# Optimization experiments

Hardware: AMD Instinct MI355X
Metric: run time of the kernel (lower is better)

The kernel has to match this reference:

```python
import jax, jax.numpy as jnp
import numpy as np

D_IN = 1024
D_OUT = 1024
NUM_HEADS = 16
HEAD_DIM = D_OUT // NUM_HEADS


def setup_inputs() -> dict:
    key = jax.random.key(0)
    ks = jax.random.split(key, 6)
    s = 0.02
    return {
        "x": jax.random.normal(ks[0], (4, 2048, D_IN), dtype=jnp.float32),
        "W_q": jax.random.normal(ks[1], (D_IN, D_OUT), dtype=jnp.float32) * s,
        "W_k": jax.random.normal(ks[2], (D_IN, D_OUT), dtype=jnp.float32) * s,
        "W_v": jax.random.normal(ks[3], (D_IN, D_OUT), dtype=jnp.float32) * s,
        "W_o": jax.random.normal(ks[4], (D_OUT, D_OUT), dtype=jnp.float32) * s,
        "b_o": jax.random.normal(ks[5], (D_OUT,), dtype=jnp.float32) * s,
    }


def reference(x, W_q, W_k, W_v, W_o, b_o):
    b, n, _ = x.shape
    # project and split heads: [b, h, n, d]
    q = (x @ W_q).reshape(b, n, NUM_HEADS, HEAD_DIM).transpose(0, 2, 1, 3)
    k = (x @ W_k).reshape(b, n, NUM_HEADS, HEAD_DIM).transpose(0, 2, 1, 3)
    v = (x @ W_v).reshape(b, n, NUM_HEADS, HEAD_DIM).transpose(0, 2, 1, 3)
    scores = jnp.einsum("bhqd,bhkd->bhqk", q, k)
    causal = jnp.tril(jnp.ones((n, n), dtype=bool))  # True = keep
    scores = jnp.where(causal, scores, -jnp.inf)
    attn = jax.nn.softmax(scores / np.sqrt(HEAD_DIM).astype(np.float32), axis=-1)
    ctx = jnp.einsum("bhqk,bhkd->bhqd", attn, v)
    ctx = ctx.transpose(0, 2, 1, 3).reshape(b, n, D_OUT)
    return ctx @ W_o + b_o
```

## Files before the change

kernel.cpp:

```cpp
#include <hip/hip_runtime.h>
#include <hip/hip_bf16.h>

#define NHEADS 16
#define HDIM 64
#define SEQ 2048
#define BATCH 4
#define DMODEL 1024
#define MTOT (BATCH * SEQ)

typedef short v8s __attribute__((ext_vector_type(8)));
typedef short v4s __attribute__((ext_vector_type(4)));
typedef float v4f __attribute__((ext_vector_type(4)));
typedef float v16f __attribute__((ext_vector_type(16)));
typedef unsigned int v4u __attribute__((ext_vector_type(4)));
typedef unsigned short u16;
typedef unsigned int u32;

__device__ __forceinline__ u16 f2bf(float f) {
    union { float f; unsigned u; } v; v.f = f;
    unsigned r = v.u + 0x7FFFu + ((v.u >> 16) & 1u);
    return (u16)(r >> 16);
}

__device__ __forceinline__ void g2l16(const u16* g, short* l) {
    __builtin_amdgcn_global_load_lds(
        (const __attribute__((address_space(1))) u32*)g,
        (__attribute__((address_space(3))) u32*)l, 16, 0, 0);
}

__device__ __forceinline__ unsigned pk_bf16(float a, float b) {
    unsigned r;
    asm("v_cvt_pk_bf16_f32 %0, %1, %2" : "=v"(r) : "v"(a), "v"(b));
    return r;
}
__device__ __forceinline__ void pl32swap(unsigned& x, unsigned& y) {
    asm("v_permlane32_swap_b32 %0, %1" : "+v"(x), "+v"(y));
}
__device__ __forceinline__ v8s build_pa(float a0, float a1, float a2, float a3,
                                        float b0, float b1, float b2, float b3) {
    unsigned X  = pk_bf16(a0, a1);
    unsigned X2 = pk_bf16(a2, a3);
    unsigned Y  = pk_bf16(b0, b1);
    unsigned Y2 = pk_bf16(b2, b3);
    pl32swap(X, Y);
    pl32swap(X2, Y2);
    v4u w; w[0] = X; w[1] = X2; w[2] = Y; w[3] = Y2;
    return __builtin_bit_cast(v8s, w);
}

__device__ __forceinline__ void transpose_body(
    const float* __restrict__ src, u16* __restrict__ dst, int k0, int n0)
{
    __shared__ __align__(8) short Ts[64 * 68];
    const int t = threadIdx.x;
    const int n4 = (t & 15) * 4, kl = t >> 4;
#pragma unroll
    for (int it = 0; it < 4; ++it) {
        int k = kl + 16 * it;
        v4f v = *(const v4f*)&src[(size_t)(k0 + k) * DMODEL + n0 + n4];
        v4s p;
#pragma unroll
        for (int e = 0; e < 4; ++e) p[e] = (short)f2bf(v[e]);
        *(v4s*)&Ts[k * 68 + n4] = p;
    }
    __syncthreads();
    const int nl = t >> 4, k4 = (t & 15) * 4;
#pragma unroll
    for (int it = 0; it < 4; ++it) {
        int n = nl + 16 * it;
        v4s o;
#pragma unroll
        for (int e = 0; e < 4; ++e) o[e] = Ts[(k4 + e) * 68 + n];
        *(v4s*)&dst[(size_t)(n0 + n) * DMODEL + k0 + k4] = o;
    }
}

__global__ __launch_bounds__(256)
void transpose_w(const float* __restrict__ src, u16* __restrict__ dst)
{
    transpose_body(src, dst, blockIdx.x * 64, blockIdx.y * 64);
}

__global__ __launch_bounds__(256)
void prep(const float* __restrict__ x, u16* __restrict__ xb,
          const float* __restrict__ s0, const float* __restrict__ s1,
          const float* __restrict__ s2, const float* __restrict__ s3,
          u16* __restrict__ wdst)
{
    const int blk = blockIdx.x;
    if (blk < 1024) {
        const int z = blk >> 8;
        const int rem = blk & 255;
        const float* src = (z == 0) ? s0 : (z == 1) ? s1 : (z == 2) ? s2 : s3;
        transpose_body(src, wdst + (size_t)z * DMODEL * DMODEL,
                       (rem & 15) * 64, (rem >> 4) * 64);
    } else {
        size_t i = ((size_t)(blk - 1024) * 256 + threadIdx.x) * 8;
        v4f a = *(const v4f*)&x[i];
        v4f b = *(const v4f*)&x[i + 4];
        v8s p;
#pragma unroll
        for (int e = 0; e < 4; ++e) p[e] = (short)f2bf(a[e]);
#pragma unroll
        for (int e = 0; e < 4; ++e) p[4 + e] = (short)f2bf(b[e]);
        *(v8s*)&xb[i] = p;
    }
}

#define QSCALE (0.125f * 1.44269504088896f)

#define QKV_ABUF (256 * 64)
#define QKV_BBUF (128 * 64)

__device__ __forceinline__ void qkv_stage3(
    const u16* __restrict__ xb, const u16* __restrict__ W,
    int m0, int t, int s, int part, short* As3, short* Bs3)
{
    const int srr = t >> 3;
    const int scol = ((t & 7) ^ (srr & 7)) * 8;
    short* A = As3 + (s % 3) * QKV_ABUF;
    short* B = Bs3 + (s % 3) * QKV_BBUF;
    const int k0 = s * 64;
    if (part == 0) {
        g2l16(&xb[(size_t)(m0 + srr) * DMODEL + k0 + scol], &A[t * 8]);
        g2l16(&xb[(size_t)(m0 + 64 + srr) * DMODEL + k0 + scol],
              &A[4096 + t * 8]);
        g2l16(&W[(size_t)srr * DMODEL + k0 + scol], &B[t * 8]);
    } else {
        g2l16(&xb[(size_t)(m0 + 128 + srr) * DMODEL + k0 + scol],
              &A[8192 + t * 8]);
        g2l16(&xb[(size_t)(m0 + 192 + srr) * DMODEL + k0 + scol],
              &A[12288 + t * 8]);
        g2l16(&W[(size_t)(64 + srr) * DMODEL + k0 + scol], &B[4096 + t * 8]);
    }
}

template <bool SW>
__device__ __forceinline__ void qkv_loop32(
    const u16* __restrict__ xb, const u16* __restrict__ W,
    int m0, int t, short* As3, short* Bs3, v16f (&acc)[2][2])
{
    const int lane = t & 63;
    const int l31 = lane & 31;
    const int hi = lane >> 5;
    const int wave = t >> 6;
    const int wm = (wave >> 1) * 64;
    const int wn = (wave & 1) * 64;
    const int x7 = l31 & 7;

    qkv_stage3(xb, W, m0, t, 0, 0, As3, Bs3);
    qkv_stage3(xb, W, m0, t, 0, 1, As3, Bs3);
    qkv_stage3(xb, W, m0, t, 1, 0, As3, Bs3);
    qkv_stage3(xb, W, m0, t, 1, 1, As3, Bs3);
    asm volatile("s_waitcnt vmcnt(6)" ::: "memory");
    __builtin_amdgcn_sched_barrier(0);
    __builtin_amdgcn_s_barrier();
    __builtin_amdgcn_sched_barrier(0);

#pragma unroll 1
    for (int tt = 0; tt < 16; ++tt) {
        const short* A = As3 + (tt % 3) * QKV_ABUF;
        const short* B = Bs3 + (tt % 3) * QKV_BBUF;
        v8s af[2][2], bf[2][2];

#pragma unroll
        for (int i = 0; i < 2; ++i)
#pragma unroll
            for (int ks = 0; ks < 2; ++ks) {
                af[i][ks] = *(const v8s*)&A[(wm + i * 32 + l31) * 64 +
                                            (((ks * 2 + hi) ^ x7) << 3)];
                bf[i][ks] = *(const v8s*)&B[(wn + i * 32 + l31) * 64 +
                                            (((ks * 2 + hi) ^ x7) << 3)];
            }
        if (tt + 2 < 16) qkv_stage3(xb, W, m0, t, tt + 2, 0, As3, Bs3);
        __builtin_amdgcn_s_barrier();
        asm volatile("s_waitcnt lgkmcnt(0)" ::: "memory");
        __builtin_amdgcn_sched_barrier(0);
        __builtin_amdgcn_s_setprio(1);
#pragma unroll
        for (int i = 0; i < 2; ++i)
#pragma unroll
            for (int j = 0; j < 2; ++j)
#pragma unroll
                for (int ks = 0; ks < 2; ++ks) {
                    if (SW)
                        acc[i][j] = __builtin_amdgcn_mfma_f32_32x32x16_bf16(
                            bf[j][ks], af[i][ks], acc[i][j], 0, 0, 0);
                    else
                        acc[i][j] = __builtin_amdgcn_mfma_f32_32x32x16_bf16(
                            af[i][ks], bf[j][ks], acc[i][j], 0, 0, 0);
                }
        __builtin_amdgcn_s_setprio(0);
        __builtin_amdgcn_s_barrier();

#pragma unroll
        for (int i = 0; i < 2; ++i)
#pragma unroll
            for (int ks = 0; ks < 2; ++ks) {
                af[i][ks] = *(const v8s*)&A[(wm + i * 32 + l31) * 64 +
                                            ((((ks + 2) * 2 + hi) ^ x7) << 3)];
                bf[i][ks] = *(const v8s*)&B[(wn + i * 32 + l31) * 64 +
                                            ((((ks + 2) * 2 + hi) ^ x7) << 3)];
            }
        if (tt + 2 < 16) qkv_stage3(xb, W, m0, t, tt + 2, 1, As3, Bs3);
        __builtin_amdgcn_s_barrier();
        asm volatile("s_waitcnt lgkmcnt(0)" ::: "memory");
        __builtin_amdgcn_sched_barrier(0);
        __builtin_amdgcn_s_setprio(1);
#pragma unroll
        for (int i = 0; i < 2; ++i)
#pragma unroll
            for (int j = 0; j < 2; ++j)
#pragma unroll
                for (int ks = 0; ks < 2; ++ks) {
                    if (SW)
                        acc[i][j] = __builtin_amdgcn_mfma_f32_32x32x16_bf16(
                            bf[j][ks], af[i][ks], acc[i][j], 0, 0, 0);
                    else
                        acc[i][j] = __builtin_amdgcn_mfma_f32_32x32x16_bf16(
                            af[i][ks], bf[j][ks], acc[i][j], 0, 0, 0);
                }
        __builtin_amdgcn_s_setprio(0);
        if (tt < 14)       asm volatile("s_waitcnt vmcnt(6)" ::: "memory");
        else if (tt == 14) asm volatile("s_waitcnt vmcnt(0)" ::: "memory");
        __builtin_amdgcn_sched_barrier(0);
        __builtin_amdgcn_s_barrier();
        __builtin_amdgcn_sched_barrier(0);
    }
}

__global__ __launch_bounds__(512, 1)
void qkv_fast(const u16* __restrict__ xb, const u16* __restrict__ Wt,
              u16* __restrict__ Qb, u16* __restrict__ Kb, u16* __restrict__ Vt)
{
    __shared__ __align__(16) short As3[3 * QKV_ABUF];
    __shared__ __align__(16) short Bs3[3 * QKV_BBUF];

    const int bx = blockIdx.x;
    const int which = bx >> 3;
    const int n0 = (bx & 7) * 128;
    const int m0 = blockIdx.y * 256;
    const u16* W = Wt + (size_t)which * DMODEL * DMODEL + (size_t)n0 * DMODEL;

    const int t = threadIdx.x;
    const int lane = t & 63;
    const int l31 = lane & 31;
    const int hi = lane >> 5;
    const int wave = t >> 6;
    const int wm = (wave >> 1) * 64;
    const int wn = (wave & 1) * 64;

    v16f acc[2][2];
#pragma unroll
    for (int i = 0; i < 2; ++i)
#pragma unroll
        for (int j = 0; j < 2; ++j)
#pragma unroll
            for (int r = 0; r < 16; ++r) acc[i][j][r] = 0.f;

    if (which == 2) {
        qkv_loop32<true>(xb, W, m0, t, As3, Bs3, acc);
#pragma unroll
        for (int i = 0; i < 2; ++i) {
            int m = m0 + wm + i * 32 + l31;
            int b = m >> 11, n = m & (SEQ - 1);
#pragma unroll
            for (int j = 0; j < 2; ++j)
#pragma unroll
                for (int r = 0; r < 16; ++r) {
                    int ncol = n0 + wn + j * 32 + (r & 3) + 8 * (r >> 2)
                               + 4 * hi;
                    int h = ncol >> 6, d = ncol & 63;
                    Vt[((size_t)(b * NHEADS + h) * HDIM + d) * SEQ + n] =
                        f2bf(acc[i][j][r]);
                }
        }
    } else {
        qkv_loop32<false>(xb, W, m0, t, As3, Bs3, acc);
        u16* Ob = which ? Kb : Qb;
        const float scale = which ? 1.0f : QSCALE;
#pragma unroll
        for (int j = 0; j < 2; ++j) {
            int col = n0 + wn + j * 32 + l31;
            int h = col >> 6, d = col & 63;
#pragma unroll
            for (int i = 0; i < 2; ++i)
#pragma unroll
                for (int r = 0; r < 16; ++r) {
                    int m = m0 + wm + i * 32 + (r & 3) + 8 * (r >> 2) + 4 * hi;
                    int b = m >> 11, n = m & (SEQ - 1);
                    Ob[((size_t)(b * NHEADS + h) * SEQ + n) * HDIM + d] =
                        f2bf(acc[i][j][r] * scale);
                }
        }
    }
}

__device__ __forceinline__ void qkv_epilogue(
    v4f (&acc)[4][4], int which, int n0, int m0, int wn, int wm,
    int l15, int quad, u16* Qb, u16* Kb, u16* Vt)
{
    if (which == 2) {
#pragma unroll
        for (int i = 0; i < 4; ++i)
#pragma unroll
            for (int j = 0; j < 4; ++j) {
                int col = n0 + wn + j * 16 + l15;
                int h = col >> 6, d = col & 63;
                int m = m0 + wm + i * 16 + quad * 4;
                int b = m >> 11, n = m & (SEQ - 1);
                v4s pv;
#pragma unroll
                for (int r = 0; r < 4; ++r) pv[r] = (short)f2bf(acc[i][j][r]);
                *(v4s*)&Vt[((size_t)(b * NHEADS + h) * HDIM + d) * SEQ + n] = pv;
            }
    } else {
        u16* Ob = (which == 0) ? Qb : Kb;
        const float scale = (which == 0) ? QSCALE : 1.0f;
#pragma unroll
        for (int i = 0; i < 4; ++i)
#pragma unroll
            for (int j = 0; j < 4; ++j) {
                int col = n0 + wn + j * 16 + l15;
                int h = col >> 6, d = col & 63;
#pragma unroll
                for (int r = 0; r < 4; ++r) {
                    int m = m0 + wm + i * 16 + quad * 4 + r;
                    int b = m >> 11, n = m & (SEQ - 1);
                    Ob[((size_t)(b * NHEADS + h) * SEQ + n) * HDIM + d] =
                        f2bf(acc[i][j][r] * scale);
                }
            }
    }
}

__global__ __launch_bounds__(256, 2)
void qkv_slow(const float* __restrict__ x, const u16* __restrict__ Wt,
              u16* __restrict__ Qb, u16* __restrict__ Kb, u16* __restrict__ Vt)
{
    __shared__ __align__(16) short As[128 * 32];
    __shared__ __align__(16) short Bs[128 * 32];

    const int which = blockIdx.z;
    const u16* W = Wt + (size_t)which * DMODEL * DMODEL;

    const int n0 = blockIdx.x * 128;
    const int m0 = blockIdx.y * 128;
    const int t = threadIdx.x;
    const int lane = t & 63;
    const int l15 = lane & 15;
    const int quad = lane >> 4;
    const int wave = t >> 6;
    const int wm = (wave >> 1) * 64;
    const int wn = (wave & 1) * 64;
    const int srow = t >> 2;
    const int sc8 = (t & 3) * 8;

    v4f acc[4][4];
#pragma unroll
    for (int i = 0; i < 4; ++i)
#pragma unroll
        for (int j = 0; j < 4; ++j) acc[i][j] = {0.f, 0.f, 0.f, 0.f};

    for (int k0 = 0; k0 < DMODEL; k0 += 32) {
        __syncthreads();
        g2l16(&W[(size_t)(n0 + srow) * DMODEL + k0 + sc8], &Bs[srow * 32 + sc8]);
        g2l16(&W[(size_t)(n0 + 64 + srow) * DMODEL + k0 + sc8],
              &Bs[(64 + srow) * 32 + sc8]);
#pragma unroll
        for (int it = 0; it < 2; ++it) {
            int row = srow + 64 * it;
            const float* xp = &x[(size_t)(m0 + row) * DMODEL + k0 + sc8];
            v4f x0 = *(const v4f*)xp;
            v4f x1 = *(const v4f*)(xp + 4);
            v8s av;
#pragma unroll
            for (int e = 0; e < 4; ++e) av[e] = (short)f2bf(x0[e]);
#pragma unroll
            for (int e = 0; e < 4; ++e) av[4 + e] = (short)f2bf(x1[e]);
            *(v8s*)&As[row * 32 + sc8] = av;
        }
        __syncthreads();

        v8s af[4], bf[4];
#pragma unroll
        for (int i = 0; i < 4; ++i)
            af[i] = *(const v8s*)&As[(wm + i * 16 + l15) * 32 + quad * 8];
#pragma unroll
        for (int j = 0; j < 4; ++j)
            bf[j] = *(const v8s*)&Bs[(wn + j * 16 + l15) * 32 + quad * 8];
#pragma unroll
        for (int i = 0; i < 4; ++i)
#pragma unroll
            for (int j = 0; j < 4; ++j)
                acc[i][j] = __builtin_amdgcn_mfma_f32_16x16x32_bf16(
                    af[i], bf[j], acc[i][j], 0, 0, 0);
    }
    qkv_epilogue(acc, which, n0, m0, wn, wm, l15, quad, Qb, Kb, Vt);
}

#define VXOR(d) ((((d) & 7) << 1) | (((d) >> 3) & 1))

__global__ __launch_bounds__(256, 2)
void attn(const u16* __restrict__ Qb, const u16* __restrict__ Kb,
          const u16* __restrict__ Vt, u16* __restrict__ Cx)
{
    __shared__ __align__(16) short Ks[2][128 * 64];
    __shared__ __align__(16) short Vs[2][64 * 128];

    const int ell = blockIdx.x;
    const int xcd = ell & 7;
    const int rest = ell >> 3;
    const int p = rest & 7;
    const int bh = ((rest >> 3) << 3) | xcd;

    const int t = threadIdx.x;
    const int lane = t & 63;
    const int l31 = lane & 31;
    const int hi = lane >> 5;
    const int wave = t >> 6;
    const int koff = hi * 8;

    const u16* Qh = Qb + (size_t)bh * SEQ * HDIM;
    const u16* Kh = Kb + (size_t)bh * SEQ * HDIM;
    const u16* Vh = Vt + (size_t)bh * HDIM * SEQ;

    const int krow = t >> 3;
    const int kslot = t & 7;
    const int vrow = t >> 4;
    const int vslot = t & 15;
    const int b = bh >> 4, h = bh & 15;

#pragma unroll 1
    for (int phase = 0; phase < 2; ++phase) {
        const int qt = phase ? p : (15 - p);
        const int q0w = qt * 128 + wave * 32;

        v8s qf[4];
#pragma unroll
        for (int dc = 0; dc < 4; ++dc)
            qf[dc] = *(const v8s*)
                &Qh[(size_t)(q0w + l31) * HDIM + dc * 16 + koff];

        v16f o0, o1;
#pragma unroll
        for (int r = 0; r < 16; ++r) { o0[r] = 0.f; o1[r] = 0.f; }
        float ls = 0.f;

        v8s pk[4], pv[4];
#pragma unroll
        for (int it = 0; it < 4; ++it)
            pk[it] = *(const v8s*)
                &Kh[(size_t)(it * 32 + krow) * HDIM + kslot * 8];
#pragma unroll
        for (int it = 0; it < 4; ++it)
            pv[it] = *(const v8s*)
                &Vh[(size_t)(it * 16 + vrow) * SEQ + vslot * 8];
#pragma unroll
        for (int it = 0; it < 4; ++it) {
            int row = it * 32 + krow;
            *(v8s*)&Ks[0][row * 64 + ((kslot ^ (row & 7)) << 3)] = pk[it];
        }
#pragma unroll
        for (int it = 0; it < 4; ++it) {
            int d = it * 16 + vrow;
            *(v8s*)&Vs[0][d * 128 + ((vslot ^ VXOR(d)) << 3)] = pv[it];
        }
        __syncthreads();

#pragma unroll 1
        for (int kb = 0; kb <= qt; ++kb) {
            const int cur = kb & 1;

            if (kb < qt) {
                const int kn = (kb + 1) * 128;
#pragma unroll
                for (int it = 0; it < 4; ++it)
                    pk[it] = *(const v8s*)
                        &Kh[(size_t)(kn + it * 32 + krow) * HDIM + kslot * 8];
#pragma unroll
                for (int it = 0; it < 4; ++it)
                    pv[it] = *(const v8s*)
                        &Vh[(size_t)(it * 16 + vrow) * SEQ + kn + vslot * 8];
            }

#pragma unroll
            for (int k2 = 0; k2 < 2; ++k2) {
                const int kbase = kb * 128 + k2 * 64;
                if (kbase > q0w + 31) continue;
                const bool diag = (kbase + 63 > q0w);
                const int qrow = q0w + l31;

                v16f st0, st1;
#pragma unroll
                for (int r = 0; r < 16; ++r) { st0[r] = 0.f; st1[r] = 0.f; }
#pragma unroll
                for (int dc = 0; dc < 4; ++dc) {
                    const int ds = dc * 2 + hi;
                    const int r0 = k2 * 64 + l31;
                    const int r1 = k2 * 64 + 32 + l31;
                    v8s kf0 = *(const v8s*)
                        &Ks[cur][r0 * 64 + ((ds ^ (r0 & 7)) << 3)];
                    v8s kf1 = *(const v8s*)
                        &Ks[cur][r1 * 64 + ((ds ^ (r1 & 7)) << 3)];
                    st0 = __builtin_amdgcn_mfma_f32_32x32x16_bf16(
                        kf0, qf[dc], st0, 0, 0, 0);
                    st1 = __builtin_amdgcn_mfma_f32_32x32x16_bf16(
                        kf1, qf[dc], st1, 0, 0, 0);
                }

                v16f pe0, pe1;
                if (!diag) {
#pragma unroll
                    for (int r = 0; r < 16; ++r) {
                        pe0[r] = exp2f(st0[r]);
                        pe1[r] = exp2f(st1[r]);
                    }
                } else {
#pragma unroll
                    for (int r = 0; r < 16; ++r) {
                        int kl = kbase + (r & 3) + 8 * (r >> 2) + 4 * hi;
                        pe0[r] = (kl > qrow) ? 0.f : exp2f(st0[r]);
                        pe1[r] = (kl + 32 > qrow) ? 0.f : exp2f(st1[r]);
                    }
                }
#pragma unroll
                for (int r = 0; r < 16; ++r) ls += pe0[r] + pe1[r];

                v8s pa0 = build_pa(pe0[0], pe0[1], pe0[2], pe0[3],
                                   pe0[4], pe0[5], pe0[6], pe0[7]);
                v8s pa1 = build_pa(pe0[8], pe0[9], pe0[10], pe0[11],
                                   pe0[12], pe0[13], pe0[14], pe0[15]);
                v8s pa2 = build_pa(pe1[0], pe1[1], pe1[2], pe1[3],
                                   pe1[4], pe1[5], pe1[6], pe1[7]);
                v8s pa3 = build_pa(pe1[8], pe1[9], pe1[10], pe1[11],
                                   pe1[12], pe1[13], pe1[14], pe1[15]);

#pragma unroll
                for (int kc = 0; kc < 4; ++kc) {
                    v8s pav = (kc == 0) ? pa0 : (kc == 1) ? pa1
                              : (kc == 2) ? pa2 : pa3;
                    const int ks = k2 * 8 + kc * 2 + hi;
                    const int d0 = l31, d1 = 32 + l31;
                    v8s vf0 = *(const v8s*)
                        &Vs[cur][d0 * 128 + ((ks ^ VXOR(d0)) << 3)];
                    v8s vf1 = *(const v8s*)
                        &Vs[cur][d1 * 128 + ((ks ^ VXOR(d1)) << 3)];
                    o0 = __builtin_amdgcn_mfma_f32_32x32x16_bf16(
                        pav, vf0, o0, 0, 0, 0);
                    o1 = __builtin_amdgcn_mfma_f32_32x32x16_bf16(
                        pav, vf1, o1, 0, 0, 0);
                }
            }

            if (kb < qt) {
#pragma unroll
                for (int it = 0; it < 4; ++it) {
                    int row = it * 32 + krow;
                    *(v8s*)&Ks[cur ^ 1][row * 64 + ((kslot ^ (row & 7)) << 3)]
                        = pk[it];
                }
#pragma unroll
                for (int it = 0; it < 4; ++it) {
                    int d = it * 16 + vrow;
                    *(v8s*)&Vs[cur ^ 1][d * 128 + ((vslot ^ VXOR(d)) << 3)]
                        = pv[it];
                }
            }
            __syncthreads();
        }

        ls += __shfl_xor(ls, 32, 64);
        float inv = 1.f / ls;
#pragma unroll
        for (int r = 0; r < 16; ++r) {
            int m = (r & 3) + 8 * (r >> 2) + 4 * hi;
            float im = __shfl(inv, m, 64);
            size_t idx = ((size_t)(b * SEQ + q0w + m)) * DMODEL
                         + h * HDIM + l31;
            Cx[idx] = f2bf(o0[r] * im);
            Cx[idx + 32] = f2bf(o1[r] * im);
        }
    }
}

__global__ __launch_bounds__(256, 2)
void out_gemm(const u16* __restrict__ Cx, const u16* __restrict__ WoT,
              const float* __restrict__ bo, float* __restrict__ Y)
{
    __shared__ __align__(16) short As[128 * 64];
    __shared__ __align__(16) short Bs[128 * 64];

    const int n0 = blockIdx.x * 128;
    const int m0 = blockIdx.y * 128;
    const int t = threadIdx.x;
    const int lane = t & 63;
    const int l15 = lane & 15;
    const int quad = lane >> 4;
    const int wave = t >> 6;
    const int wm = (wave >> 1) * 64;
    const int wn = (wave & 1) * 64;
    const int srow = t >> 3;
    const int sc8 = (t & 7) * 8;

    v4f acc[4][4];
#pragma unroll
    for (int i = 0; i < 4; ++i)
#pragma unroll
        for (int j = 0; j < 4; ++j) acc[i][j] = {0.f, 0.f, 0.f, 0.f};

    for (int k0 = 0; k0 < DMODEL; k0 += 64) {
        __syncthreads();
#pragma unroll
        for (int c = 0; c < 4; ++c) {
            g2l16(&Cx[(size_t)(m0 + c * 32 + srow) * DMODEL + k0 + sc8],
                  &As[(c * 32 + srow) * 64 + sc8]);
            g2l16(&WoT[(size_t)(n0 + c * 32 + srow) * DMODEL + k0 + sc8],
                  &Bs[(c * 32 + srow) * 64 + sc8]);
        }
        __syncthreads();

#pragma unroll
        for (int kh = 0; kh < 2; ++kh) {
            v8s af[4], bf[4];
#pragma unroll
            for (int i = 0; i < 4; ++i)
                af[i] = *(const v8s*)
                    &As[(wm + i * 16 + l15) * 64 + kh * 32 + quad * 8];
#pragma unroll
            for (int j = 0; j < 4; ++j)
                bf[j] = *(const v8s*)
                    &Bs[(wn + j * 16 + l15) * 64 + kh * 32 + quad * 8];
#pragma unroll
            for (int i = 0; i < 4; ++i)
#pragma unroll
                for (int j = 0; j < 4; ++j)
                    acc[i][j] = __builtin_amdgcn_mfma_f32_16x16x32_bf16(
                        af[i], bf[j], acc[i][j], 0, 0, 0);
        }
    }

#pragma unroll
    for (int i = 0; i < 4; ++i)
#pragma unroll
        for (int j = 0; j < 4; ++j) {
            int col = n0 + wn + j * 16 + l15;
            float bias = bo[col];
#pragma unroll
            for (int r = 0; r < 4; ++r) {
                int m = m0 + wm + i * 16 + quad * 4 + r;
                Y[(size_t)m * DMODEL + col] = acc[i][j][r] + bias;
            }
        }
}

extern "C" void kernel_launch(void* const* d_in, const int* in_sizes, int n_in,
                              void* d_out, int out_size, void* d_ws,
                              size_t ws_size, hipStream_t stream)
{
    const float* x  = (const float*)d_in[0];
    const float* Wq = (const float*)d_in[1];
    const float* Wk = (const float*)d_in[2];
    const float* Wv = (const float*)d_in[3];
    const float* Wo = (const float*)d_in[4];
    const float* bo = (const float*)d_in[5];
    float* Y = (float*)d_out;

    const size_t per = (size_t)BATCH * NHEADS * SEQ * HDIM;
    const size_t wsz = (size_t)DMODEL * DMODEL;
    u16* base = (u16*)d_ws;

    if (ws_size >= (size_t)72 * 1024 * 1024) {
        u16* xb  = base;
        u16* Cx  = base;
        u16* Wt4 = base + per;
        u16* Qb  = base + per + 4 * wsz;
        u16* Kb  = Qb + per;
        u16* Vt  = Kb + per;

        prep<<<1024 + MTOT * DMODEL / (256 * 8), 256, 0, stream>>>(
            x, xb, Wq, Wk, Wv, Wo, Wt4);
        qkv_fast<<<dim3(24, MTOT / 256), 512, 0, stream>>>(
            xb, Wt4, Qb, Kb, Vt);
        attn<<<512, 256, 0, stream>>>(Qb, Kb, Vt, Cx);
        out_gemm<<<dim3(DMODEL / 128, MTOT / 128), 256, 0, stream>>>(
            Cx, Wt4 + 3 * wsz, bo, Y);
    } else {
        u16* Wt  = base;
        u16* Cx  = base;
        u16* Qb  = base + per;
        u16* WoT = base + per;
        u16* Kb  = base + 2 * per;
        u16* Vt  = base + 3 * per;

        transpose_w<<<dim3(16, 16), 256, 0, stream>>>(Wq, Wt);
        transpose_w<<<dim3(16, 16), 256, 0, stream>>>(Wk, Wt + wsz);
        transpose_w<<<dim3(16, 16), 256, 0, stream>>>(Wv, Wt + 2 * wsz);
        qkv_slow<<<dim3(DMODEL / 128, MTOT / 128, 3), 256, 0, stream>>>(
            x, Wt, Qb, Kb, Vt);
        attn<<<512, 256, 0, stream>>>(Qb, Kb, Vt, Cx);
        transpose_w<<<dim3(16, 16), 256, 0, stream>>>(Wo, WoT);
        out_gemm<<<dim3(DMODEL / 128, MTOT / 128), 256, 0, stream>>>(
            Cx, WoT, bo, Y);
    }
}
```

Before: 265.8 us.

## Split attention into one query tile per block with single-buffered LDS

The attention kernel no longer pairs two causal query tiles per block. It launches 1024 blocks, each handling one query tile, with a new ordering of tiles across blocks meant to balance causal work. The K/V shared-memory buffers go from double to single buffering, halving LDS use, and launch bounds rise to 4 blocks per SIMD for higher occupancy. In exchange it adds an extra barrier per key block, loses the LDS double-buffer overlap (register prefetch remains), and load balance now depends on the hardware scheduler.

```diff
diff --git a/kernel.cpp b/kernel.cpp
--- a/kernel.cpp
+++ b/kernel.cpp
@@ -401,18 +401,20 @@
 
 #define VXOR(d) ((((d) & 7) << 1) | (((d) >> 3) & 1))
 
-__global__ __launch_bounds__(256, 2)
+__global__ __launch_bounds__(256, 4)
 void attn(const u16* __restrict__ Qb, const u16* __restrict__ Kb,
           const u16* __restrict__ Vt, u16* __restrict__ Cx)
 {
-    __shared__ __align__(16) short Ks[2][128 * 64];
-    __shared__ __align__(16) short Vs[2][64 * 128];
+    __shared__ __align__(16) short Ks[128 * 64];
+    __shared__ __align__(16) short Vs[64 * 128];
 
     const int ell = blockIdx.x;
     const int xcd = ell & 7;
     const int rest = ell >> 3;
-    const int p = rest & 7;
-    const int bh = ((rest >> 3) << 3) | xcd;
+    const int bh = ((rest & 7) << 3) | xcd;
+    const int tix = rest >> 3;
+    const int tk = tix >> 2, tt_ = tix & 3;
+    const int qt = 4 * tk + ((tt_ + tk) & 3);
 
     const int t = threadIdx.x;
     const int lane = t & 63;
@@ -431,156 +433,129 @@
     const int vslot = t & 15;
     const int b = bh >> 4, h = bh & 15;
 
+    const int q0w = qt * 128 + wave * 32;
+
+    v8s qf[4];
+#pragma unroll
+    for (int dc = 0; dc < 4; ++dc)
+        qf[dc] = *(const v8s*)
+            &Qh[(size_t)(q0w + l31) * HDIM + dc * 16 + koff];
+
+    v16f o0, o1;
+#pragma unroll
+    for (int r = 0; r < 16; ++r) { o0[r] = 0.f; o1[r] = 0.f; }
+    float ls = 0.f;
+
+    v8s pk[4], pv[4];
+#pragma unroll
+    for (int it = 0; it < 4; ++it)
+        pk[it] = *(const v8s*)&Kh[(size_t)(it * 32 + krow) * HDIM + kslot * 8];
+#pragma unroll
+    for (int it = 0; it < 4; ++it)
+        pv[it] = *(const v8s*)&Vh[(size_t)(it * 16 + vrow) * SEQ + vslot * 8];
+
 #pragma unroll 1
-    for (int phase = 0; phase < 2; ++phase) {
-        const int qt = phase ? p : (15 - p);
-        const int q0w = qt * 128 + wave * 32;
-
-        v8s qf[4];
-#pragma unroll
-        for (int dc = 0; dc < 4; ++dc)
-            qf[dc] = *(const v8s*)
-                &Qh[(size_t)(q0w + l31) * HDIM + dc * 16 + koff];
-
-        v16f o0, o1;
-#pragma unroll
-        for (int r = 0; r < 16; ++r) { o0[r] = 0.f; o1[r] = 0.f; }
-        float ls = 0.f;
-
-        v8s pk[4], pv[4];
-#pragma unroll
-        for (int it = 0; it < 4; ++it)
-            pk[it] = *(const v8s*)
-                &Kh[(size_t)(it * 32 + krow) * HDIM + kslot * 8];
-#pragma unroll
-        for (int it = 0; it < 4; ++it)
-            pv[it] = *(const v8s*)
-                &Vh[(size_t)(it * 16 + vrow) * SEQ + vslot * 8];
+    for (int kb = 0; kb <= qt; ++kb) {
+        __syncthreads();
 #pragma unroll
         for (int it = 0; it < 4; ++it) {
             int row = it * 32 + krow;
-            *(v8s*)&Ks[0][row * 64 + ((kslot ^ (row & 7)) << 3)] = pk[it];
+            *(v8s*)&Ks[row * 64 + ((kslot ^ (row & 7)) << 3)] = pk[it];
         }
 #pragma unroll
         for (int it = 0; it < 4; ++it) {
             int d = it * 16 + vrow;
-            *(v8s*)&Vs[0][d * 128 + ((vslot ^ VXOR(d)) << 3)] = pv[it];
+            *(v8s*)&Vs[d * 128 + ((vslot ^ VXOR(d)) << 3)] = pv[it];
         }
         __syncthreads();
 
-#pragma unroll 1
-        for (int kb = 0; kb <= qt; ++kb) {
-            const int cur = kb & 1;
-
-            if (kb < qt) {
-                const int kn = (kb + 1) * 128;
-#pragma unroll
-                for (int it = 0; it < 4; ++it)
-                    pk[it] = *(const v8s*)
-                        &Kh[(size_t)(kn + it * 32 + krow) * HDIM + kslot * 8];
-#pragma unroll
-                for (int it = 0; it < 4; ++it)
-                    pv[it] = *(const v8s*)
-                        &Vh[(size_t)(it * 16 + vrow) * SEQ + kn + vslot * 8];
-            }
-
-#pragma unroll
-            for (int k2 = 0; k2 < 2; ++k2) {
-                const int kbase = kb * 128 + k2 * 64;
-                if (kbase > q0w + 31) continue;
-                const bool diag = (kbase + 63 > q0w);
-                const int qrow = q0w + l31;
-
-                v16f st0, st1;
-#pragma unroll
-                for (int r = 0; r < 16; ++r) { st0[r] = 0.f; st1[r] = 0.f; }
-#pragma unroll
-                for (int dc = 0; dc < 4; ++dc) {
-                    const int ds = dc * 2 + hi;
-                    const int r0 = k2 * 64 + l31;
-                    const int r1 = k2 * 64 + 32 + l31;
-                    v8s kf0 = *(const v8s*)
-                        &Ks[cur][r0 * 64 + ((ds ^ (r0 & 7)) << 3)];
-                    v8s kf1 = *(const v8s*)
-                        &Ks[cur][r1 * 64 + ((ds ^ (r1 & 7)) << 3)];
-                    st0 = __builtin_amdgcn_mfma_f32_32x32x16_bf16(
-                        kf0, qf[dc], st0, 0, 0, 0);
-                    st1 = __builtin_amdgcn_mfma_f32_32x32x16_bf16(
-                        kf1, qf[dc], st1, 0, 0, 0);
+        if (kb < qt) {
+            const int kn = (kb + 1) * 128;
+#pragma unroll
+            for (int it = 0; it < 4; ++it)
+                pk[it] = *(const v8s*)
+                    &Kh[(size_t)(kn + it * 32 + krow) * HDIM + kslot * 8];
+#pragma unroll
+            for (int it = 0; it < 4; ++it)
+                pv[it] = *(const v8s*)
+                    &Vh[(size_t)(it * 16 + vrow) * SEQ + kn + vslot * 8];
+        }
+
+#pragma unroll
+        for (int k2 = 0; k2 < 2; ++k2) {
+            const int kbase = kb * 128 + k2 * 64;
+            if (kbase > q0w + 31) continue;
+            const bool diag = (kbase + 63 > q0w);
+            const int qrow = q0w + l31;
+
+            v16f st0, st1;
+#pragma unroll
+            for (int r = 0; r < 16; ++r) { st0[r] = 0.f; st1[r] = 0.f; }
+#pragma unroll
+            for (int dc = 0; dc < 4; ++dc) {
+                const int ds = dc * 2 + hi;
+                const int r0 = k2 * 64 + l31;
+                const int r1 = k2 * 64 + 32 + l31;
+                v8s kf0 = *(const v8s*)&Ks[r0 * 64 + ((ds ^ (r0 & 7)) << 3)];
+                v8s kf1 = *(const v8s*)&Ks[r1 * 64 + ((ds ^ (r1 & 7)) << 3)];
+                st0 = __builtin_amdgcn_mfma_f32_32x32x16_bf16(
+                    kf0, qf[dc], st0, 0, 0, 0);
+                st1 = __builtin_amdgcn_mfma_f32_32x32x16_bf16(
+                    kf1, qf[dc], st1, 0, 0, 0);
+            }
+
+            v16f pe0, pe1;
+            if (!diag) {
+#pragma unroll
+                for (int r = 0; r < 16; ++r) {
+                    pe0[r] = exp2f(st0[r]);
+                    pe1[r] = exp2f(st1[r]);
                 }
-
-                v16f pe0, pe1;
-                if (!diag) {
-#pragma unroll
-                    for (int r = 0; r < 16; ++r) {
-                        pe0[r] = exp2f(st0[r]);
-                        pe1[r] = exp2f(st1[r]);
-                    }
-                } else {
-#pragma unroll
-                    for (int r = 0; r < 16; ++r) {
-                        int kl = kbase + (r & 3) + 8 * (r >> 2) + 4 * hi;
-                        pe0[r] = (kl > qrow) ? 0.f : exp2f(st0[r]);
-                        pe1[r] = (kl + 32 > qrow) ? 0.f : exp2f(st1[r]);
-                    }
+            } else {
+#pragma unroll
+                for (int r = 0; r < 16; ++r) {
+                    int kl = kbase + (r & 3) + 8 * (r >> 2) + 4 * hi;
+                    pe0[r] = (kl > qrow) ? 0.f : exp2f(st0[r]);
+                    pe1[r] = (kl + 32 > qrow) ? 0.f : exp2f(st1[r]);
                 }
-#pragma unroll
-                for (int r = 0; r < 16; ++r) ls += pe0[r] + pe1[r];
-
-                v8s pa0 = build_pa(pe0[0], pe0[1], pe0[2], pe0[3],
-                                   pe0[4], pe0[5], pe0[6], pe0[7]);
-                v8s pa1 = build_pa(pe0[8], pe0[9], pe0[10], pe0[11],
-                                   pe0[12], pe0[13], pe0[14], pe0[15]);
-                v8s pa2 = build_pa(pe1[0], pe1[1], pe1[2], pe1[3],
-                                   pe1[4], pe1[5], pe1[6], pe1[7]);
-                v8s pa3 = build_pa(pe1[8], pe1[9], pe1[10], pe1[11],
-                                   pe1[12], pe1[13], pe1[14], pe1[15]);
-
-#pragma unroll
-                for (int kc = 0; kc < 4; ++kc) {
-                    v8s pav = (kc == 0) ? pa0 : (kc == 1) ? pa1
-                              : (kc == 2) ? pa2 : pa3;
-                    const int ks = k2 * 8 + kc * 2 + hi;
-                    const int d0 = l31, d1 = 32 + l31;
-                    v8s vf0 = *(const v8s*)
-                        &Vs[cur][d0 * 128 + ((ks ^ VXOR(d0)) << 3)];
-                    v8s vf1 = *(const v8s*)
-                        &Vs[cur][d1 * 128 + ((ks ^ VXOR(d1)) << 3)];
-                    o0 = __builtin_amdgcn_mfma_f32_32x32x16_bf16(
-                        pav, vf0, o0, 0, 0, 0);
-                    o1 = __builtin_amdgcn_mfma_f32_32x32x16_bf16(
-                        pav, vf1, o1, 0, 0, 0);
-                }
-            }
-
-            if (kb < qt) {
-#pragma unroll
-                for (int it = 0; it < 4; ++it) {
-                    int row = it * 32 + krow;
-                    *(v8s*)&Ks[cur ^ 1][row * 64 + ((kslot ^ (row & 7)) << 3)]
-                        = pk[it];
-                }
-#pragma unroll
-                for (int it = 0; it < 4; ++it) {
-                    int d = it * 16 + vrow;
-                    *(v8s*)&Vs[cur ^ 1][d * 128 + ((vslot ^ VXOR(d)) << 3)]
-                        = pv[it];
-                }
-            }
-            __syncthreads();
-        }
-
-        ls += __shfl_xor(ls, 32, 64);
-        float inv = 1.f / ls;
-#pragma unroll
-        for (int r = 0; r < 16; ++r) {
-            int m = (r & 3) + 8 * (r >> 2) + 4 * hi;
-            float im = __shfl(inv, m, 64);
-            size_t idx = ((size_t)(b * SEQ + q0w + m)) * DMODEL
-                         + h * HDIM + l31;
-            Cx[idx] = f2bf(o0[r] * im);
-            Cx[idx + 32] = f2bf(o1[r] * im);
-        }
+            }
+#pragma unroll
+            for (int r = 0; r < 16; ++r) ls += pe0[r] + pe1[r];
+
+            v8s pa0 = build_pa(pe0[0], pe0[1], pe0[2], pe0[3],
+                               pe0[4], pe0[5], pe0[6], pe0[7]);
+            v8s pa1 = build_pa(pe0[8], pe0[9], pe0[10], pe0[11],
+                               pe0[12], pe0[13], pe0[14], pe0[15]);
+            v8s pa2 = build_pa(pe1[0], pe1[1], pe1[2], pe1[3],
+                               pe1[4], pe1[5], pe1[6], pe1[7]);
+            v8s pa3 = build_pa(pe1[8], pe1[9], pe1[10], pe1[11],
+                               pe1[12], pe1[13], pe1[14], pe1[15]);
+
+#pragma unroll
+            for (int kc = 0; kc < 4; ++kc) {
+                v8s pav = (kc == 0) ? pa0 : (kc == 1) ? pa1
+                          : (kc == 2) ? pa2 : pa3;
+                const int ks = k2 * 8 + kc * 2 + hi;
+                const int d0 = l31, d1 = 32 + l31;
+                v8s vf0 = *(const v8s*)&Vs[d0 * 128 + ((ks ^ VXOR(d0)) << 3)];
+                v8s vf1 = *(const v8s*)&Vs[d1 * 128 + ((ks ^ VXOR(d1)) << 3)];
+                o0 = __builtin_amdgcn_mfma_f32_32x32x16_bf16(
+                    pav, vf0, o0, 0, 0, 0);
+                o1 = __builtin_amdgcn_mfma_f32_32x32x16_bf16(
+                    pav, vf1, o1, 0, 0, 0);
+            }
+        }
+    }
+
+    ls += __shfl_xor(ls, 32, 64);
+    float inv = 1.f / ls;
+#pragma unroll
+    for (int r = 0; r < 16; ++r) {
+        int m = (r & 3) + 8 * (r >> 2) + 4 * hi;
+        float im = __shfl(inv, m, 64);
+        size_t idx = ((size_t)(b * SEQ + q0w + m)) * DMODEL + h * HDIM + l31;
+        Cx[idx] = f2bf(o0[r] * im);
+        Cx[idx + 32] = f2bf(o1[r] * im);
     }
 }
 
@@ -682,7 +657,7 @@
             x, xb, Wq, Wk, Wv, Wo, Wt4);
         qkv_fast<<<dim3(24, MTOT / 256), 512, 0, stream>>>(
             xb, Wt4, Qb, Kb, Vt);
-        attn<<<512, 256, 0, stream>>>(Qb, Kb, Vt, Cx);
+        attn<<<1024, 256, 0, stream>>>(Qb, Kb, Vt, Cx);
         out_gemm<<<dim3(DMODEL / 128, MTOT / 128), 256, 0, stream>>>(
             Cx, Wt4 + 3 * wsz, bo, Y);
     } else {
@@ -698,7 +673,7 @@
         transpose_w<<<dim3(16, 16), 256, 0, stream>>>(Wv, Wt + 2 * wsz);
         qkv_slow<<<dim3(DMODEL / 128, MTOT / 128, 3), 256, 0, stream>>>(
             x, Wt, Qb, Kb, Vt);
-        attn<<<512, 256, 0, stream>>>(Qb, Kb, Vt, Cx);
+        attn<<<1024, 256, 0, stream>>>(Qb, Kb, Vt, Cx);
         transpose_w<<<dim3(16, 16), 256, 0, stream>>>(Wo, WoT);
         out_gemm<<<dim3(DMODEL / 128, MTOT / 128), 256, 0, stream>>>(
             Cx, WoT, bo, Y);
```

After: 328.3 us. 23.5% more time.
